# Performance work log

Measured on AMD Instinct MI355X. Metric: run time of the kernel, lower is better.

Reference implementation:

```python
import jax, jax.numpy as jnp
import numpy as np
jax.config.update("jax_enable_x64", True)  # hashing uses int64 primes as in torch

N_PTS = 1048576
L, T, F = 16, 2 ** 18, 2
N_MIN, N_MAX = 16, 1024
HID, OUT = 64, 3


def setup_inputs() -> dict:
    key = jax.random.key(0)
    ks = jax.random.split(key, 6)
    X = jax.random.uniform(ks[0], (N_PTS, 2), dtype=jnp.float32)
    hash_table = jax.random.uniform(ks[1], (L, T, F), dtype=jnp.float32,
                                    minval=-1e-4, maxval=1e-4)
    def lin(k, fan_in, fan_out):
        bound = 1.0 / np.sqrt(fan_in)
        kw, kb = jax.random.split(k)
        W = jax.random.uniform(kw, (fan_in, fan_out), dtype=jnp.float32,
                               minval=-bound, maxval=bound)
        b = jax.random.uniform(kb, (fan_out,), dtype=jnp.float32,
                               minval=-bound, maxval=bound)
        return W, b
    W1, b1 = lin(ks[2], L * F, HID)
    W2, b2 = lin(ks[3], HID, HID)
    W3, b3 = lin(ks[4], HID, HID)
    W4, b4 = lin(ks[5], HID, OUT)
    return {"X": X, "hash_table": hash_table,
            "W1": W1, "b1": b1, "W2": W2, "b2": b2,
            "W3": W3, "b3": b3, "W4": W4, "b4": b4}


def reference(X, hash_table, W1, b1, W2, b2, W3, b3, W4, b4):
    Lh, Th, Fh = hash_table.shape
    # per-level resolutions: floor(N_min * b**l), b geometric between N_min and N_max
    b_geo = np.exp((np.log(N_MAX) - np.log(N_MIN)) / (Lh - 1))
    N_values = jnp.floor(jnp.asarray(N_MIN * b_geo ** np.arange(Lh),
                                     dtype=jnp.float32))  # (L,)

    x_scaled = X[:, :, None] * N_values[None, None, :]        # (N, 2, L)
    x_floor = jnp.floor(x_scaled)

    # NOTE: original code MULTIPLIES floor coords by the 0/1 vertex pattern
    # (not add) -- we replicate that math faithfully.
    vertices = jnp.array([[0., 0., 1., 1.], [0., 1., 0., 1.]],
                         dtype=jnp.float32)                   # (2, 4)
    x_vert = (x_floor[:, :, :, None] * vertices[None, :, None, :]
              ).astype(jnp.int64)                             # (N, 2, L, 4)

    primes = jnp.array([1, 2654435761], dtype=jnp.int64)
    hv = x_vert * primes[None, :, None, None]
    x_hash = jnp.remainder(jnp.bitwise_xor(hv[:, 0], hv[:, 1]), Th)  # (N, L, 4)

    # irregular gather: per-level hash table lookup -> (N, L, 4, F)
    lookup = hash_table[jnp.arange(Lh)[None, :, None], x_hash]

    w = x_scaled - x_floor                                    # (N, 2, L)
    fx, fy = w[:, 0, :], w[:, 1, :]
    cx, cy = 1.0 - fx, 1.0 - fy
    f_stack = jnp.stack([cx * cy, cx * fy, fx * cy, fx * fy], axis=2)  # (N, L, 4)

    x_interp = jnp.sum(f_stack[:, :, :, None] * lookup, axis=2)  # (N, L, F)
    feat = x_interp.reshape(-1, Lh * Fh).astype(jnp.float32)     # (N, 32)

    h = jax.nn.leaky_relu(feat @ W1 + b1)
    h = jax.nn.leaky_relu(h @ W2 + b2)
    h = jax.nn.leaky_relu(h @ W3 + b3)
    return jax.nn.relu(h @ W4 + b4)
```

## Files before the change

kernel.cpp:

```cpp
#include <hip/hip_runtime.h>
#include <math.h>

typedef _Float16 half8  __attribute__((ext_vector_type(8)));
typedef float    float4v __attribute__((ext_vector_type(4)));

constexpr int T_ = 1 << 18;
constexpr unsigned TMASK = T_ - 1;
constexpr unsigned PRIME = 2654435761u;
constexpr int HP = 72;

constexpr int WFRAG_HALFS = 22 * 64 * 8;
constexpr int BIAS_FLOATS = 208;
constexpr int WS_BYTES    = 22528 + 240 * 4;
constexpr int WS_UINT4    = WS_BYTES / 16;
constexpr int V12_OFF     = 23488;

constexpr int BLK   = 256;
constexpr int WAVES = 4;
constexpr int PTS_PER_BLOCK = 512;

struct Meta { float n[16]; float off[16]; };

__global__ void prep_weights(const float* __restrict__ W1, const float* __restrict__ b1,
                             const float* __restrict__ W2, const float* __restrict__ b2,
                             const float* __restrict__ W3, const float* __restrict__ b3,
                             const float* __restrict__ W4, const float* __restrict__ b4,
                             const float2* __restrict__ table,
                             _Float16* __restrict__ wsW, float* __restrict__ wsB,
                             uint2* __restrict__ wsV, Meta mv)
{
    const int tid = threadIdx.x;
    const int bid = blockIdx.x;
    if (bid < 44) {
        const int e = bid * 256 + tid;
        const int frag = e >> 9;
        const int l    = (e >> 3) & 63;
        const int j    = e & 7;
        const int g = l >> 4, m = l & 15;
        float v;
        if (frag < 4) {
            v = W1[(8*g + j) * 64 + 16*frag + m];
        } else if (frag < 12) {
            const int s = (frag - 4) >> 2, t = (frag - 4) & 3;
            v = W2[(32*s + 8*g + j) * 64 + 16*t + m];
        } else if (frag < 20) {
            const int s = (frag - 12) >> 2, t = (frag - 12) & 3;
            v = W3[(32*s + 8*g + j) * 64 + 16*t + m];
        } else {
            const int s = frag - 20;
            v = (m < 3) ? W4[(32*s + 8*g + j) * 3 + m] : 0.f;
        }
        wsW[e] = (_Float16)v;
    } else if (bid == 44) {
        if (tid < 64) { wsB[tid] = b1[tid]; wsB[64 + tid] = b2[tid]; wsB[128 + tid] = b3[tid]; }
        else if (tid < 80)  { const int r = tid - 64; wsB[192 + r] = (r < 3) ? b4[r] : 0.f; }
        else if (tid < 96)  wsB[BIAS_FLOATS + (tid - 80)] = mv.n[tid - 80];
        else if (tid < 112) wsB[BIAS_FLOATS + 16 + (tid - 96)] = mv.off[tid - 96];
    } else {
        const int e = (bid - 45) * 256 + tid;
        const int total = (int)mv.off[15] + (int)mv.n[15] + 1;
        if (e < total) {
            int l = 0;
            #pragma unroll
            for (int k = 1; k < 16; ++k) if (e >= (int)mv.off[k]) l = k;
            const int i = e - (int)mv.off[l];
            const float2* tl = table + (size_t)l * T_;
            const float2 b = tl[((unsigned)i * PRIME) & TMASK];
            const float2 a = tl[i];
            union { _Float16 h[2]; unsigned u; } p0, p1;
            p0.h[0] = (_Float16)b.x; p0.h[1] = (_Float16)b.y;
            p1.h[0] = (_Float16)a.x; p1.h[1] = (_Float16)a.y;
            wsV[e] = uint2{p0.u, p1.u};
        }
    }
}

#define DS_FENCE() __asm__ volatile("s_waitcnt lgkmcnt(0)" ::: "memory")

struct Gather {
    float2   v3[4];
    unsigned v1[4];
    unsigned v2[4];
};

__device__ __forceinline__ void issue_gather(Gather& G, const float2 xy,
                                             const float2* __restrict__ table,
                                             const unsigned* __restrict__ gV12,
                                             const float (&nvq)[4], const int (&offq)[4],
                                             const int g)
{
    #pragma unroll
    for (int q = 0; q < 4; ++q) {
        const float n = nvq[q];
        const float xs = xy.x * n, ys = xy.y * n;
        const int xi = (int)floorf(xs);
        const int yi = (int)floorf(ys);
        const unsigned yp = (unsigned)yi * PRIME;
        G.v3[q] = table[(size_t)(4*g + q) * T_ + (((unsigned)xi ^ yp) & TMASK)];
        G.v1[q] = gV12[2*(offq[q] + yi) + 0];
        G.v2[q] = gV12[2*(offq[q] + xi) + 1];
    }
}

__device__ __forceinline__ half8 make_feat(const float2 xy, const Gather& G,
                                           const float (&nvq)[4],
                                           const float2 (&v0c)[4])
{
    half8 feat;
    #pragma unroll
    for (int q = 0; q < 4; ++q) {
        const float n = nvq[q];
        const float xs = xy.x * n, ys = xy.y * n;
        const float xf = floorf(xs), yf = floorf(ys);
        const float fx = xs - xf, fy = ys - yf;
        union { unsigned u; _Float16 h[2]; } u1, u2;
        u1.u = G.v1[q]; u2.u = G.v2[q];
        const float cx = 1.f - fx, cy = 1.f - fy;
        const float w0 = cx*cy, w1 = cx*fy, w2 = fx*cy, w3 = fx*fy;
        feat[2*q+0] = (_Float16)(w0*v0c[q].x + w1*(float)u1.h[0] + w2*(float)u2.h[0] + w3*G.v3[q].x);
        feat[2*q+1] = (_Float16)(w0*v0c[q].y + w1*(float)u1.h[1] + w2*(float)u2.h[1] + w3*G.v3[q].y);
    }
    return feat;
}

__device__ __forceinline__ void act_store(_Float16* __restrict__ H, const int c,
                                          const int g, const int t, const float4v acc)
{
    union { _Float16 h[4]; float2 f2; } u;
    #pragma unroll
    for (int r = 0; r < 4; ++r) {
        const float v = acc[r];
        u.h[r] = (_Float16)(v > 0.f ? v : 0.01f * v);
    }
    *(float2*)(H + c*HP + 16*t + 4*g) = u.f2;
}

__global__ __launch_bounds__(BLK)
void fused_hashnerf_mfma(const float2* __restrict__ X,
                         const float2* __restrict__ table,
                         const uint4* __restrict__ ws,
                         float* __restrict__ out)
{
    __shared__ uint4    sRaw[WS_UINT4];
    __shared__ _Float16 sH[WAVES][16 * HP];

    const int tid = threadIdx.x;
    for (int i = tid; i < WS_UINT4; i += BLK) sRaw[i] = ws[i];
    __syncthreads();

    const _Float16* Wl = (const _Float16*)sRaw;
    const float*    Bl = (const float*)(sRaw + (22528 / 16));
    const unsigned* gV12 = (const unsigned*)((const char*)ws + V12_OFF);

    const int wave = tid >> 6, lane = tid & 63;
    const int g = lane >> 4, c = lane & 15;
    _Float16* H = &sH[wave][0];

    float4v b1f[4], b2f[4], b3f[4], b4f;
    #pragma unroll
    for (int t = 0; t < 4; ++t) {
        b1f[t] = *(const float4v*)(Bl +       16*t + 4*g);
        b2f[t] = *(const float4v*)(Bl +  64 + 16*t + 4*g);
        b3f[t] = *(const float4v*)(Bl + 128 + 16*t + 4*g);
    }
    b4f = *(const float4v*)(Bl + 192 + 4*g);
    float nvq[4];
    int   offq[4];
    #pragma unroll
    for (int q = 0; q < 4; ++q) {
        nvq[q]  = Bl[BIAS_FLOATS + 4*g + q];
        offq[q] = (int)Bl[BIAS_FLOATS + 16 + 4*g + q];
    }

    const int base_pt = blockIdx.x * PTS_PER_BLOCK + wave * 128;

    float2 xy[8];
    #pragma unroll
    for (int it = 0; it < 8; ++it) xy[it] = X[base_pt + it*16 + c];

    float2 v0c[4];
    #pragma unroll
    for (int q = 0; q < 4; ++q) v0c[q] = table[(size_t)(4*g + q) * T_];

    Gather GA, GB;
    issue_gather(GA, xy[0], table, gV12, nvq, offq, g);

    #pragma unroll
    for (int it = 0; it < 8; ++it) {
        Gather& Gc = (it & 1) ? GB : GA;
        Gather& Gn = (it & 1) ? GA : GB;

        const half8 feat = make_feat(xy[it], Gc, nvq, v0c);

        if (it < 7) issue_gather(Gn, xy[it+1], table, gV12, nvq, offq, g);
        __builtin_amdgcn_sched_barrier(0);

        float4v acc[4];
        #pragma unroll
        for (int t = 0; t < 4; ++t) {
            const half8 wf = *(const half8*)(Wl + (t*64 + lane)*8);
            acc[t] = __builtin_amdgcn_mfma_f32_16x16x32_f16(wf, feat, b1f[t], 0, 0, 0);
        }
        #pragma unroll
        for (int t = 0; t < 4; ++t) act_store(H, c, g, t, acc[t]);
        DS_FENCE();

        half8 a0 = *(const half8*)(H + c*HP +      8*g);
        half8 a1 = *(const half8*)(H + c*HP + 32 + 8*g);
        #pragma unroll
        for (int t = 0; t < 4; ++t) {
            const half8 w0f = *(const half8*)(Wl + ((4 + t)*64 + lane)*8);
            const half8 w1f = *(const half8*)(Wl + ((8 + t)*64 + lane)*8);
            float4v a = __builtin_amdgcn_mfma_f32_16x16x32_f16(w0f, a0, b2f[t], 0, 0, 0);
            acc[t]    = __builtin_amdgcn_mfma_f32_16x16x32_f16(w1f, a1, a,      0, 0, 0);
        }
        #pragma unroll
        for (int t = 0; t < 4; ++t) act_store(H, c, g, t, acc[t]);
        DS_FENCE();

        a0 = *(const half8*)(H + c*HP +      8*g);
        a1 = *(const half8*)(H + c*HP + 32 + 8*g);
        #pragma unroll
        for (int t = 0; t < 4; ++t) {
            const half8 w0f = *(const half8*)(Wl + ((12 + t)*64 + lane)*8);
            const half8 w1f = *(const half8*)(Wl + ((16 + t)*64 + lane)*8);
            float4v a = __builtin_amdgcn_mfma_f32_16x16x32_f16(w0f, a0, b3f[t], 0, 0, 0);
            acc[t]    = __builtin_amdgcn_mfma_f32_16x16x32_f16(w1f, a1, a,      0, 0, 0);
        }
        #pragma unroll
        for (int t = 0; t < 4; ++t) act_store(H, c, g, t, acc[t]);
        DS_FENCE();

        a0 = *(const half8*)(H + c*HP +      8*g);
        a1 = *(const half8*)(H + c*HP + 32 + 8*g);
        const half8 w40 = *(const half8*)(Wl + (20*64 + lane)*8);
        const half8 w41 = *(const half8*)(Wl + (21*64 + lane)*8);
        float4v o = __builtin_amdgcn_mfma_f32_16x16x32_f16(w40, a0, b4f, 0, 0, 0);
        o         = __builtin_amdgcn_mfma_f32_16x16x32_f16(w41, a1, o,   0, 0, 0);
        if (g == 0) {
            float* op = out + (size_t)3 * (base_pt + it * 16 + c);
            op[0] = fmaxf(o[0], 0.f);
            op[1] = fmaxf(o[1], 0.f);
            op[2] = fmaxf(o[2], 0.f);
        }
    }
}

extern "C" void kernel_launch(void* const* d_in, const int* in_sizes, int n_in,
                              void* d_out, int out_size, void* d_ws, size_t ws_size,
                              hipStream_t stream) {
    const float2* X     = (const float2*)d_in[0];
    const float2* table = (const float2*)d_in[1];
    const float*  W1    = (const float*)d_in[2];
    const float*  b1    = (const float*)d_in[3];
    const float*  W2    = (const float*)d_in[4];
    const float*  b2    = (const float*)d_in[5];
    const float*  W3    = (const float*)d_in[6];
    const float*  b3    = (const float*)d_in[7];
    const float*  W4    = (const float*)d_in[8];
    const float*  b4    = (const float*)d_in[9];
    float* out          = (float*)d_out;

    const int npts = in_sizes[0] / 2;

    Meta mv;
    const double bg = exp((log(1024.0) - log(16.0)) / 15.0);
    int acc = 0;
    for (int l = 0; l < 16; ++l) {
        const float nl = floorf((float)(16.0 * pow(bg, (double)l)));
        mv.n[l]   = nl;
        mv.off[l] = (float)acc;
        acc += (int)nl + 1;
    }

    _Float16* wsW = (_Float16*)d_ws;
    float*    wsB = (float*)((char*)d_ws + 22528);
    uint2*    wsV = (uint2*)((char*)d_ws + V12_OFF);

    prep_weights<<<62, 256, 0, stream>>>(W1, b1, W2, b2, W3, b3, W4, b4, table,
                                         wsW, wsB, wsV, mv);
    fused_hashnerf_mfma<<<npts / PTS_PER_BLOCK, BLK, 0, stream>>>(X, table, (const uint4*)d_ws, out);
}
```

Before: 219.5 us.

## Keep MLP activations in registers via permuted weight layout; deepen gather prefetch

The weight fragments for layers 2-4 are reordered along the K dimension so that each MFMA output accumulator can be fed directly as the next layer's B operand. This removes the per-layer LDS store, lgkm wait and reload of activations. The hash-table gather is also triple-buffered, prefetching two points ahead instead of one, to hide more gather latency. The deeper prefetch raises register pressure, which could lower occupancy.

```diff
diff --git a/kernel.cpp b/kernel.cpp
--- a/kernel.cpp
+++ b/kernel.cpp
@@ -7,7 +7,6 @@
 constexpr int T_ = 1 << 18;
 constexpr unsigned TMASK = T_ - 1;
 constexpr unsigned PRIME = 2654435761u;
-constexpr int HP = 72;
 
 constexpr int WFRAG_HALFS = 22 * 64 * 8;
 constexpr int BIAS_FLOATS = 208;
@@ -16,7 +15,6 @@
 constexpr int V12_OFF     = 23488;
 
 constexpr int BLK   = 256;
-constexpr int WAVES = 4;
 constexpr int PTS_PER_BLOCK = 512;
 
 struct Meta { float n[16]; float off[16]; };
@@ -37,23 +35,24 @@
         const int l    = (e >> 3) & 63;
         const int j    = e & 7;
         const int g = l >> 4, m = l & 15;
+        const int u = j >> 2, r = j & 3;
         float v;
         if (frag < 4) {
             v = W1[(8*g + j) * 64 + 16*frag + m];
         } else if (frag < 12) {
             const int s = (frag - 4) >> 2, t = (frag - 4) & 3;
-            v = W2[(32*s + 8*g + j) * 64 + 16*t + m];
+            v = W2[(32*s + 16*u + 4*g + r) * 64 + 16*t + m];
         } else if (frag < 20) {
             const int s = (frag - 12) >> 2, t = (frag - 12) & 3;
-            v = W3[(32*s + 8*g + j) * 64 + 16*t + m];
+            v = W3[(32*s + 16*u + 4*g + r) * 64 + 16*t + m];
         } else {
             const int s = frag - 20;
-            v = (m < 3) ? W4[(32*s + 8*g + j) * 3 + m] : 0.f;
+            v = (m < 3) ? W4[(32*s + 16*u + 4*g + r) * 3 + m] : 0.f;
         }
         wsW[e] = (_Float16)v;
     } else if (bid == 44) {
         if (tid < 64) { wsB[tid] = b1[tid]; wsB[64 + tid] = b2[tid]; wsB[128 + tid] = b3[tid]; }
-        else if (tid < 80)  { const int r = tid - 64; wsB[192 + r] = (r < 3) ? b4[r] : 0.f; }
+        else if (tid < 80)  { const int r2 = tid - 64; wsB[192 + r2] = (r2 < 3) ? b4[r2] : 0.f; }
         else if (tid < 96)  wsB[BIAS_FLOATS + (tid - 80)] = mv.n[tid - 80];
         else if (tid < 112) wsB[BIAS_FLOATS + 16 + (tid - 96)] = mv.off[tid - 96];
     } else {
@@ -75,8 +74,6 @@
     }
 }
 
-#define DS_FENCE() __asm__ volatile("s_waitcnt lgkmcnt(0)" ::: "memory")
-
 struct Gather {
     float2   v3[4];
     unsigned v1[4];
@@ -123,16 +120,17 @@
     return feat;
 }
 
-__device__ __forceinline__ void act_store(_Float16* __restrict__ H, const int c,
-                                          const int g, const int t, const float4v acc)
-{
-    union { _Float16 h[4]; float2 f2; } u;
-    #pragma unroll
-    for (int r = 0; r < 4; ++r) {
-        const float v = acc[r];
-        u.h[r] = (_Float16)(v > 0.f ? v : 0.01f * v);
-    }
-    *(float2*)(H + c*HP + 16*t + 4*g) = u.f2;
+__device__ __forceinline__ void repack(const float4v (&acc)[4], half8& a0, half8& a1)
+{
+    #pragma unroll
+    for (int u = 0; u < 2; ++u)
+        #pragma unroll
+        for (int r = 0; r < 4; ++r) {
+            const float v0 = acc[u][r];
+            const float v1 = acc[2 + u][r];
+            a0[4*u + r] = (_Float16)(v0 > 0.f ? v0 : 0.01f * v0);
+            a1[4*u + r] = (_Float16)(v1 > 0.f ? v1 : 0.01f * v1);
+        }
 }
 
 __global__ __launch_bounds__(BLK)
@@ -141,8 +139,7 @@
                          const uint4* __restrict__ ws,
                          float* __restrict__ out)
 {
-    __shared__ uint4    sRaw[WS_UINT4];
-    __shared__ _Float16 sH[WAVES][16 * HP];
+    __shared__ uint4 sRaw[WS_UINT4];
 
     const int tid = threadIdx.x;
     for (int i = tid; i < WS_UINT4; i += BLK) sRaw[i] = ws[i];
@@ -154,7 +151,6 @@
 
     const int wave = tid >> 6, lane = tid & 63;
     const int g = lane >> 4, c = lane & 15;
-    _Float16* H = &sH[wave][0];
 
     float4v b1f[4], b2f[4], b3f[4], b4f;
     #pragma unroll
@@ -182,17 +178,18 @@
     #pragma unroll
     for (int q = 0; q < 4; ++q) v0c[q] = table[(size_t)(4*g + q) * T_];
 
-    Gather GA, GB;
-    issue_gather(GA, xy[0], table, gV12, nvq, offq, g);
+    Gather G0, G1, G2;
+    issue_gather(G0, xy[0], table, gV12, nvq, offq, g);
+    issue_gather(G1, xy[1], table, gV12, nvq, offq, g);
 
     #pragma unroll
     for (int it = 0; it < 8; ++it) {
-        Gather& Gc = (it & 1) ? GB : GA;
-        Gather& Gn = (it & 1) ? GA : GB;
+        Gather& Gc = (it % 3 == 0) ? G0 : (it % 3 == 1) ? G1 : G2;
+        Gather& Gn = ((it + 2) % 3 == 0) ? G0 : ((it + 2) % 3 == 1) ? G1 : G2;
 
         const half8 feat = make_feat(xy[it], Gc, nvq, v0c);
 
-        if (it < 7) issue_gather(Gn, xy[it+1], table, gV12, nvq, offq, g);
+        if (it < 6) issue_gather(Gn, xy[it+2], table, gV12, nvq, offq, g);
         __builtin_amdgcn_sched_barrier(0);
 
         float4v acc[4];
@@ -201,12 +198,9 @@
             const half8 wf = *(const half8*)(Wl + (t*64 + lane)*8);
             acc[t] = __builtin_amdgcn_mfma_f32_16x16x32_f16(wf, feat, b1f[t], 0, 0, 0);
         }
-        #pragma unroll
-        for (int t = 0; t < 4; ++t) act_store(H, c, g, t, acc[t]);
-        DS_FENCE();
-
-        half8 a0 = *(const half8*)(H + c*HP +      8*g);
-        half8 a1 = *(const half8*)(H + c*HP + 32 + 8*g);
+
+        half8 a0, a1;
+        repack(acc, a0, a1);
         #pragma unroll
         for (int t = 0; t < 4; ++t) {
             const half8 w0f = *(const half8*)(Wl + ((4 + t)*64 + lane)*8);
@@ -214,12 +208,8 @@
             float4v a = __builtin_amdgcn_mfma_f32_16x16x32_f16(w0f, a0, b2f[t], 0, 0, 0);
             acc[t]    = __builtin_amdgcn_mfma_f32_16x16x32_f16(w1f, a1, a,      0, 0, 0);
         }
-        #pragma unroll
-        for (int t = 0; t < 4; ++t) act_store(H, c, g, t, acc[t]);
-        DS_FENCE();
-
-        a0 = *(const half8*)(H + c*HP +      8*g);
-        a1 = *(const half8*)(H + c*HP + 32 + 8*g);
+
+        repack(acc, a0, a1);
         #pragma unroll
         for (int t = 0; t < 4; ++t) {
             const half8 w0f = *(const half8*)(Wl + ((12 + t)*64 + lane)*8);
@@ -227,12 +217,8 @@
             float4v a = __builtin_amdgcn_mfma_f32_16x16x32_f16(w0f, a0, b3f[t], 0, 0, 0);
             acc[t]    = __builtin_amdgcn_mfma_f32_16x16x32_f16(w1f, a1, a,      0, 0, 0);
         }
-        #pragma unroll
-        for (int t = 0; t < 4; ++t) act_store(H, c, g, t, acc[t]);
-        DS_FENCE();
-
-        a0 = *(const half8*)(H + c*HP +      8*g);
-        a1 = *(const half8*)(H + c*HP + 32 + 8*g);
+
+        repack(acc, a0, a1);
         const half8 w40 = *(const half8*)(Wl + (20*64 + lane)*8);
         const half8 w41 = *(const half8*)(Wl + (21*64 + lane)*8);
         float4v o = __builtin_amdgcn_mfma_f32_16x16x32_f16(w40, a0, b4f, 0, 0, 0);
```

Result: no change. 222.5 us (+1.4%).
